# Kernel tuning notes

Hardware: AMD Instinct MI355X
Metric: run time of the kernel (lower is better)

## Reference

```python
import jax, jax.numpy as jnp
import numpy as np

N = 512        # n_t (sequence length of observations)
D_IN = 128     # input feature dim
PROJ = 128     # proj_dim
ENC = 128      # enc_dim
H = 4          # num_head
E = PROJ // H  # per-head dim = 32
SCALE = 1.0 / np.float32(np.sqrt(E))


def setup_inputs() -> dict:
    key = jax.random.key(0)
    ks = jax.random.split(key, 14)
    g = lambda k, sh: (jax.random.normal(k, sh, jnp.float32) * 0.05)
    inp = jax.random.normal(ks[0], (N, D_IN), jnp.float32)
    # irregular observation times, sorted ascending
    pos = jnp.sort(jax.random.uniform(ks[1], (N,), jnp.float32) * 100.0)
    # PosEncodingBlock frequency vector f: exp(arange(0,enc,2) * -(ln(10000)/enc))
    f = jnp.exp(jnp.arange(0, ENC, 2, dtype=jnp.float32) * (-(np.log(10000.0) / ENC)))
    return {
        "inp": inp, "pos": pos, "f": f,
        "Wq": g(ks[2], (D_IN, PROJ)), "bq": g(ks[3], (PROJ,)),
        "Wk": g(ks[4], (D_IN, PROJ)), "bk": g(ks[5], (PROJ,)),
        "Wv": g(ks[6], (D_IN, PROJ)), "bv": g(ks[7], (PROJ,)),
        "Wqt": g(ks[8], (D_IN, PROJ)), "bqt": g(ks[9], (PROJ,)),
        "Wt": g(ks[10], (ENC, PROJ)), "bt": g(ks[11], (PROJ,)),
    }


def _heads(x):
    # 'n (h e) -> h n e'
    return x.reshape(N, H, E).transpose(1, 0, 2)


def reference(inp, pos, f, Wq, bq, Wk, bk, Wv, bv, Wqt, bqt, Wt, bt):
    q = _heads(inp @ Wq + bq)   # (h, n, e)
    k = _heads(inp @ Wk + bk)
    v = _heads(inp @ Wv + bv)
    qt = _heads(inp @ Wqt + bqt)

    score = jnp.einsum('hne,hme->hnm', q, k) * SCALE  # (h, n, n)

    # Equivariant relative-time positional encoding: (n, n, ENC)
    rel_time = pos[:, None] - pos[None, :]                    # (n, n)
    angles = rel_time[..., None] * f                          # (n, n, ENC/2)
    # rearrange([sin, cos], 'z t l k -> t l (k z)') interleaves sin/cos per freq
    pos_enc = jnp.stack([jnp.sin(angles), jnp.cos(angles)], axis=-1).reshape(N, N, ENC)

    # time_dense then 'n1 n2 (h e) -> h n1 n2 e'
    t = (pos_enc @ Wt + bt).reshape(N, N, H, E).transpose(2, 0, 1, 3)  # (h, n, n, e)
    # tf.linalg.matvec(t, q_t): bias[h,i,j] = sum_e t[h,i,j,e] * qt[h,i,e]
    score = score + jnp.einsum('hnme,hne->hnm', t, qt) * SCALE

    mask = jnp.tril(jnp.ones((N, N), dtype=bool))
    score = jnp.where(mask, score, -jnp.inf)
    weight = jax.nn.softmax(score, axis=-1)
    weight = jnp.where(mask, weight, 0.0)
    # dropout is identity at inference

    out = jnp.einsum('hnm,hme->hne', weight, v)  # (h, n, e)
    return out.transpose(1, 0, 2).reshape(N, PROJ)  # 'h n e -> n (h e)'
```

## Files before the change

### kernel.cpp

```cpp
#include <hip/hip_runtime.h>
#include <math.h>

namespace {
constexpr int N = 512;
constexpr int DIN = 128;
constexpr int PROJ = 128;
constexpr int H = 4;
constexpr int E = 32;
constexpr int KF = 64;
constexpr int FEAT = E + 2*KF;
constexpr float SCALE = 0.17677669529663687f;
constexpr int TI = 8;
constexpr int JQ = 8;
constexpr int CHUNK = 64;
}

__device__ __forceinline__ float wave_max(float v) {
  #pragma unroll
  for (int o = 32; o > 0; o >>= 1) v = fmaxf(v, __shfl_xor(v, o, 64));
  return v;
}
__device__ __forceinline__ float wave_sum(float v) {
  #pragma unroll
  for (int o = 32; o > 0; o >>= 1) v += __shfl_xor(v, o, 64);
  return v;
}

__global__ __launch_bounds__(256)
void proj_feat_kernel(const float* __restrict__ inp,
                      const float* __restrict__ pos, const float* __restrict__ f,
                      const float* __restrict__ Wq, const float* __restrict__ bq,
                      const float* __restrict__ Wk, const float* __restrict__ bk,
                      const float* __restrict__ Wv, const float* __restrict__ bv,
                      const float* __restrict__ Wqt, const float* __restrict__ bqt,
                      const float* __restrict__ Wt, const float* __restrict__ bt,
                      float* __restrict__ Afeat, float* __restrict__ BTk,
                      float* __restrict__ Vmat, float* __restrict__ Btrig,
                      float* __restrict__ c0)
{
  const int bx = blockIdx.x;
  const int t = threadIdx.x;
  const int c = t & 127;

  if (bx < 384) {
    const int mat = bx >> 7, rowTile = bx & 127;
    const int i0 = rowTile * 4;
    const int half = t >> 7;
    __shared__ float x[4][DIN];
    #pragma unroll
    for (int r = 0; r < 2; ++r) {
      const int id = t + r * 256;
      x[id >> 7][id & 127] = inp[i0 * DIN + id];
    }
    const float* W; const float* bvec;
    switch (mat) {
      case 0:  W = Wq; bvec = bq; break;
      case 1:  W = Wk; bvec = bk; break;
      default: W = Wv; bvec = bv; break;
    }
    __syncthreads();
    const int r0 = half * 2, r1 = r0 + 1;
    float a0 = 0.f, a1 = 0.f;
    #pragma unroll 8
    for (int d = 0; d < DIN; d += 2) {
      const float w0 = W[d * PROJ + c];
      const float w1 = W[(d + 1) * PROJ + c];
      const float2 x0 = *(const float2*)&x[r0][d];
      const float2 x1 = *(const float2*)&x[r1][d];
      a0 += w0 * x0.x + w1 * x0.y;
      a1 += w0 * x1.x + w1 * x1.y;
    }
    const float bb = bvec[c];
    a0 += bb; a1 += bb;
    const int h = c >> 5, e = c & 31;
    const int row0 = i0 + r0, row1 = i0 + r1;
    if (mat == 0) {
      Afeat[(h * N + row0) * FEAT + e] = a0;
      Afeat[(h * N + row1) * FEAT + e] = a1;
    } else if (mat == 1) {
      BTk[(size_t)(h * E + e) * N + row0] = a0;
      BTk[(size_t)(h * E + e) * N + row1] = a1;
    } else {
      Vmat[(h * N + row0) * E + e] = a0;
      Vmat[(h * N + row1) * E + e] = a1;
    }
    return;
  }

  const int i0 = (bx - 384) * 2;
  const int r = t >> 7;
  __shared__ float x[2][DIN];
  __shared__ float qt_l[2][PROJ];
  __shared__ float ss[2][KF], sc[2][KF];
  __shared__ float ul[2][H][PROJ];

  x[r][c] = inp[i0 * DIN + t];
  if (t < 128) {
    const int rr = t >> 6, k = t & 63;
    float s_, c_;
    sincosf(pos[i0 + rr] * f[k], &s_, &c_);
    ss[rr][k] = s_; sc[rr][k] = c_;
  }
  __syncthreads();

  {
    float a = 0.f;
    #pragma unroll 8
    for (int d = 0; d < DIN; d += 2) {
      const float w0 = Wqt[d * PROJ + c];
      const float w1 = Wqt[(d + 1) * PROJ + c];
      const float2 xv = *(const float2*)&x[r][d];
      a += w0 * xv.x + w1 * xv.y;
    }
    qt_l[r][c] = a + bqt[c];
  }
  __syncthreads();

  {
    const int g = t >> 7;
    const float* wrow = &Wt[c * PROJ];
    #pragma unroll
    for (int hh = 2 * g; hh < 2 * g + 2; ++hh) {
      float uA = 0.f, uB = 0.f;
      #pragma unroll
      for (int e4 = 0; e4 < E; e4 += 4) {
        const float4 w = *(const float4*)&wrow[hh * E + e4];
        const float4 qA = *(const float4*)&qt_l[0][hh * E + e4];
        const float4 qB = *(const float4*)&qt_l[1][hh * E + e4];
        uA += w.x * qA.x + w.y * qA.y + w.z * qA.z + w.w * qA.w;
        uB += w.x * qB.x + w.y * qB.y + w.z * qB.z + w.w * qB.w;
      }
      ul[0][hh][c] = uA;
      ul[1][hh][c] = uB;
    }
  }
  if (t < 8) {
    const int rr = t & 1, hh = t >> 1;
    float acc = 0.f;
    for (int e2 = 0; e2 < E; ++e2) acc += bt[hh * E + e2] * qt_l[rr][hh * E + e2];
    c0[hh * N + i0 + rr] = acc;
  }
  __syncthreads();

  {
    const int k = t & 63, hh = t >> 6;
    #pragma unroll
    for (int rr = 0; rr < 2; ++rr) {
      const float u0 = ul[rr][hh][2 * k], u1 = ul[rr][hh][2 * k + 1];
      const float s_ = ss[rr][k], c_ = sc[rr][k];
      Afeat[(hh * N + i0 + rr) * FEAT + E + k]      =  u0 * s_ + u1 * c_;
      Afeat[(hh * N + i0 + rr) * FEAT + E + KF + k] = -u0 * c_ + u1 * s_;
      if (hh == 0) {
        Btrig[k * N + i0 + rr]        = c_;
        Btrig[(KF + k) * N + i0 + rr] = s_;
      }
    }
  }
}

__global__ __launch_bounds__(256, 4)
void attn_partial(const float* __restrict__ Afeat, const float* __restrict__ BTk,
                  const float* __restrict__ Btrig, const float* __restrict__ Vmat,
                  const float* __restrict__ c0,
                  float* __restrict__ Po, float* __restrict__ Pm,
                  float* __restrict__ Ps)
{
  const int b = blockIdx.x, h = blockIdx.y, q = blockIdx.z;
  const int i0 = b * TI, jbase = q * CHUNK;
  if (jbase > i0) return;
  const int t = threadIdx.x;
  const int lane = t & 63;
  const int rh = __builtin_amdgcn_readfirstlane(t >> 6);
  const int j = jbase + lane;

  __shared__ float pT[CHUNK][12];
  __shared__ float obuf[16][TI][32];

  const float* A0 = Afeat + (size_t)(h * N + i0 + rh * 2) * FEAT;
  const float* A1 = A0 + FEAT;
  const float cc0 = c0[h * N + i0 + rh * 2];
  const float cc1 = c0[h * N + i0 + rh * 2 + 1];

  float acc0 = 0.f, acc1 = 0.f;
  {
    const float* Bk = BTk + (size_t)h * E * N + j;
    const float* Bt = Btrig + j;
    #pragma unroll
    for (int bb = 0; bb < 10; ++bb) {
      const float* src = (bb < 2) ? (Bk + (size_t)(bb * 16) * N)
                                  : (Bt + (size_t)((bb - 2) * 16) * N);
      const int aoff = 16 * bb;
      float bv[16];
      #pragma unroll
      for (int dd = 0; dd < 16; ++dd) bv[dd] = src[(size_t)dd * N];
      #pragma unroll
      for (int dd = 0; dd < 16; dd += 4) {
        const float4 a0 = *(const float4*)&A0[aoff + dd];
        const float4 a1 = *(const float4*)&A1[aoff + dd];
        acc0 += a0.x * bv[dd] + a0.y * bv[dd+1] + a0.z * bv[dd+2] + a0.w * bv[dd+3];
        acc1 += a1.x * bv[dd] + a1.y * bv[dd+1] + a1.z * bv[dd+2] + a1.w * bv[dd+3];
      }
    }
  }

  const int i_0 = i0 + rh * 2, i_1 = i_0 + 1;
  const float s0 = (j <= i_0) ? (acc0 + cc0) * SCALE : -INFINITY;
  const float s1 = (j <= i_1) ? (acc1 + cc1) * SCALE : -INFINITY;

  const float m0 = wave_max(s0);
  const float m1 = wave_max(s1);
  const float p0 = __expf(s0 - m0);
  const float p1 = __expf(s1 - m1);
  const float sum0 = wave_sum(p0);
  const float sum1 = wave_sum(p1);

  *(float2*)&pT[lane][rh * 2] = make_float2(p0, p1);
  if (lane == 0) {
    const int base = (h * N + i_0) * JQ + q;
    Pm[base]      = m0; Ps[base]      = sum0;
    Pm[base + JQ] = m1; Ps[base + JQ] = sum1;
  }
  __syncthreads();

  const int e2 = (t & 15) * 2, gg = t >> 4;
  float2 o[TI];
  #pragma unroll
  for (int r = 0; r < TI; ++r) o[r] = make_float2(0.f, 0.f);
  const float* Vh = Vmat + ((size_t)h * N + jbase) * E + e2;
  #pragma unroll
  for (int it = 0; it < CHUNK / 16; ++it) {
    const int jl = gg + 16 * it;
    const float2 vv = *(const float2*)&Vh[jl * E];
    const float4 pa = *(const float4*)&pT[jl][0];
    const float4 pb = *(const float4*)&pT[jl][4];
    o[0].x += pa.x * vv.x; o[0].y += pa.x * vv.y;
    o[1].x += pa.y * vv.x; o[1].y += pa.y * vv.y;
    o[2].x += pa.z * vv.x; o[2].y += pa.z * vv.y;
    o[3].x += pa.w * vv.x; o[3].y += pa.w * vv.y;
    o[4].x += pb.x * vv.x; o[4].y += pb.x * vv.y;
    o[5].x += pb.y * vv.x; o[5].y += pb.y * vv.y;
    o[6].x += pb.z * vv.x; o[6].y += pb.z * vv.y;
    o[7].x += pb.w * vv.x; o[7].y += pb.w * vv.y;
  }
  #pragma unroll
  for (int r = 0; r < TI; ++r) *(float2*)&obuf[gg][r][e2] = o[r];
  __syncthreads();
  {
    const int r = t >> 5, e = t & 31;
    float tot = 0.f;
    #pragma unroll
    for (int g2 = 0; g2 < 16; ++g2) tot += obuf[g2][r][e];
    Po[((size_t)(h * N + i0 + r) * JQ + q) * E + e] = tot;
  }
}

__global__ __launch_bounds__(256)
void attn_combine(const float* __restrict__ Po, const float* __restrict__ Pm,
                  const float* __restrict__ Ps, float* __restrict__ out)
{
  const int gid = blockIdx.x * 256 + threadIdx.x;
  const int task = gid >> 5, e = gid & 31;
  const int h = task >> 9, i = task & (N - 1);
  const int nq = (i >> 6) + 1;
  float m = -INFINITY;
  for (int qq = 0; qq < nq; ++qq) m = fmaxf(m, Pm[task * JQ + qq]);
  float s = 0.f, o = 0.f;
  for (int qq = 0; qq < nq; ++qq) {
    const float w = __expf(Pm[task * JQ + qq] - m);
    s += Ps[task * JQ + qq] * w;
    o += Po[(size_t)(task * JQ + qq) * E + e] * w;
  }
  out[i * PROJ + h * E + e] = o / s;
}

extern "C" void kernel_launch(void* const* d_in, const int* in_sizes, int n_in,
                              void* d_out, int out_size, void* d_ws, size_t ws_size,
                              hipStream_t stream) {
  const float* inp = (const float*)d_in[0];
  const float* pos = (const float*)d_in[1];
  const float* f   = (const float*)d_in[2];
  const float* Wq  = (const float*)d_in[3];
  const float* bq  = (const float*)d_in[4];
  const float* Wk  = (const float*)d_in[5];
  const float* bk  = (const float*)d_in[6];
  const float* Wv  = (const float*)d_in[7];
  const float* bv  = (const float*)d_in[8];
  const float* Wqt = (const float*)d_in[9];
  const float* bqt = (const float*)d_in[10];
  const float* Wt  = (const float*)d_in[11];
  const float* bt  = (const float*)d_in[12];
  float* out = (float*)d_out;

  float* ws    = (float*)d_ws;
  float* Afeat = ws;
  float* BTk   = Afeat + H * N * FEAT;
  float* Btrig = BTk + (size_t)H * E * N;
  float* Vmat  = Btrig + 2 * KF * N;
  float* c0    = Vmat + H * N * E;
  float* Po    = c0 + H * N;
  float* Pm    = Po + (size_t)H * N * JQ * E;
  float* Ps    = Pm + H * N * JQ;

  proj_feat_kernel<<<640, 256, 0, stream>>>(inp, pos, f, Wq, bq, Wk, bk, Wv, bv,
                                            Wqt, bqt, Wt, bt,
                                            Afeat, BTk, Vmat, Btrig, c0);
  attn_partial<<<dim3(N / TI, H, JQ), 256, 0, stream>>>(Afeat, BTk, Btrig, Vmat,
                                                        c0, Po, Pm, Ps);
  attn_combine<<<H * N * E / 256, 256, 0, stream>>>(Po, Pm, Ps, out);
}
```

Baseline: 30.64 us.

## Split score dot product over feature segments per wave and merge B features

Each wave in the score phase now covers all 8 query rows over one quarter of the 160-wide feature dimension instead of 2 rows over the full dimension. The partial sums are reduced through shared memory. The K and trig feature tables are merged into one per-head Bfeat buffer, so each B element loaded from global memory is reused across 8 rows instead of 2. The trig rows are now duplicated per head, which adds workspace and writes. The change also adds a sync and LDS traffic and drops the occupancy hint from launch bounds.

```diff
diff --git a/kernel.cpp b/kernel.cpp
--- a/kernel.cpp
+++ b/kernel.cpp
@@ -13,6 +13,7 @@
 constexpr int TI = 8;
 constexpr int JQ = 8;
 constexpr int CHUNK = 64;
+constexpr int FSEG = FEAT / 4;
 }
 
 __device__ __forceinline__ float wave_max(float v) {
@@ -34,9 +35,8 @@
                       const float* __restrict__ Wv, const float* __restrict__ bv,
                       const float* __restrict__ Wqt, const float* __restrict__ bqt,
                       const float* __restrict__ Wt, const float* __restrict__ bt,
-                      float* __restrict__ Afeat, float* __restrict__ BTk,
-                      float* __restrict__ Vmat, float* __restrict__ Btrig,
-                      float* __restrict__ c0)
+                      float* __restrict__ Afeat, float* __restrict__ Bfeat,
+                      float* __restrict__ Vmat, float* __restrict__ c0)
 {
   const int bx = blockIdx.x;
   const int t = threadIdx.x;
@@ -78,8 +78,8 @@
       Afeat[(h * N + row0) * FEAT + e] = a0;
       Afeat[(h * N + row1) * FEAT + e] = a1;
     } else if (mat == 1) {
-      BTk[(size_t)(h * E + e) * N + row0] = a0;
-      BTk[(size_t)(h * E + e) * N + row1] = a1;
+      Bfeat[(size_t)(h * FEAT + e) * N + row0] = a0;
+      Bfeat[(size_t)(h * FEAT + e) * N + row1] = a1;
     } else {
       Vmat[(h * N + row0) * E + e] = a0;
       Vmat[(h * N + row1) * E + e] = a1;
@@ -150,18 +150,15 @@
       const float s_ = ss[rr][k], c_ = sc[rr][k];
       Afeat[(hh * N + i0 + rr) * FEAT + E + k]      =  u0 * s_ + u1 * c_;
       Afeat[(hh * N + i0 + rr) * FEAT + E + KF + k] = -u0 * c_ + u1 * s_;
-      if (hh == 0) {
-        Btrig[k * N + i0 + rr]        = c_;
-        Btrig[(KF + k) * N + i0 + rr] = s_;
-      }
-    }
-  }
-}
-
-__global__ __launch_bounds__(256, 4)
-void attn_partial(const float* __restrict__ Afeat, const float* __restrict__ BTk,
-                  const float* __restrict__ Btrig, const float* __restrict__ Vmat,
-                  const float* __restrict__ c0,
+      Bfeat[(size_t)(hh * FEAT + E + k) * N + i0 + rr]      = c_;
+      Bfeat[(size_t)(hh * FEAT + E + KF + k) * N + i0 + rr] = s_;
+    }
+  }
+}
+
+__global__ __launch_bounds__(256)
+void attn_partial(const float* __restrict__ Afeat, const float* __restrict__ Bfeat,
+                  const float* __restrict__ Vmat, const float* __restrict__ c0,
                   float* __restrict__ Po, float* __restrict__ Pm,
                   float* __restrict__ Ps)
 {
@@ -170,42 +167,46 @@
   if (jbase > i0) return;
   const int t = threadIdx.x;
   const int lane = t & 63;
-  const int rh = __builtin_amdgcn_readfirstlane(t >> 6);
+  const int w = __builtin_amdgcn_readfirstlane(t >> 6);
   const int j = jbase + lane;
 
+  __shared__ float pacc[4][TI][65];
   __shared__ float pT[CHUNK][12];
   __shared__ float obuf[16][TI][32];
 
-  const float* A0 = Afeat + (size_t)(h * N + i0 + rh * 2) * FEAT;
-  const float* A1 = A0 + FEAT;
-  const float cc0 = c0[h * N + i0 + rh * 2];
-  const float cc1 = c0[h * N + i0 + rh * 2 + 1];
-
-  float acc0 = 0.f, acc1 = 0.f;
-  {
-    const float* Bk = BTk + (size_t)h * E * N + j;
-    const float* Bt = Btrig + j;
-    #pragma unroll
-    for (int bb = 0; bb < 10; ++bb) {
-      const float* src = (bb < 2) ? (Bk + (size_t)(bb * 16) * N)
-                                  : (Bt + (size_t)((bb - 2) * 16) * N);
-      const int aoff = 16 * bb;
-      float bv[16];
+  {
+    const float* Arow = Afeat + (size_t)(h * N + i0) * FEAT + FSEG * w;
+    const float* Bp   = Bfeat + ((size_t)h * FEAT + FSEG * w) * N + j;
+    float acc[TI];
+    #pragma unroll
+    for (int r = 0; r < TI; ++r) acc[r] = 0.f;
+    #pragma unroll
+    for (int dd = 0; dd < FSEG; dd += 4) {
+      const float b0 = Bp[(size_t)(dd + 0) * N];
+      const float b1 = Bp[(size_t)(dd + 1) * N];
+      const float b2 = Bp[(size_t)(dd + 2) * N];
+      const float b3 = Bp[(size_t)(dd + 3) * N];
       #pragma unroll
-      for (int dd = 0; dd < 16; ++dd) bv[dd] = src[(size_t)dd * N];
-      #pragma unroll
-      for (int dd = 0; dd < 16; dd += 4) {
-        const float4 a0 = *(const float4*)&A0[aoff + dd];
-        const float4 a1 = *(const float4*)&A1[aoff + dd];
-        acc0 += a0.x * bv[dd] + a0.y * bv[dd+1] + a0.z * bv[dd+2] + a0.w * bv[dd+3];
-        acc1 += a1.x * bv[dd] + a1.y * bv[dd+1] + a1.z * bv[dd+2] + a1.w * bv[dd+3];
+      for (int r = 0; r < TI; ++r) {
+        const float4 a = *(const float4*)&Arow[r * FEAT + dd];
+        acc[r] += a.x * b0 + a.y * b1 + a.z * b2 + a.w * b3;
       }
     }
-  }
-
-  const int i_0 = i0 + rh * 2, i_1 = i_0 + 1;
-  const float s0 = (j <= i_0) ? (acc0 + cc0) * SCALE : -INFINITY;
-  const float s1 = (j <= i_1) ? (acc1 + cc1) * SCALE : -INFINITY;
+    #pragma unroll
+    for (int r = 0; r < TI; ++r) pacc[w][r][lane] = acc[r];
+  }
+  __syncthreads();
+
+  const int i_0 = i0 + 2 * w, i_1 = i_0 + 1;
+  const float cc0 = c0[h * N + i_0];
+  const float cc1 = c0[h * N + i_1];
+  const float d0 = pacc[0][2 * w][lane] + pacc[1][2 * w][lane]
+                 + pacc[2][2 * w][lane] + pacc[3][2 * w][lane];
+  const float d1 = pacc[0][2 * w + 1][lane] + pacc[1][2 * w + 1][lane]
+                 + pacc[2][2 * w + 1][lane] + pacc[3][2 * w + 1][lane];
+
+  const float s0 = (j <= i_0) ? (d0 + cc0) * SCALE : -INFINITY;
+  const float s1 = (j <= i_1) ? (d1 + cc1) * SCALE : -INFINITY;
 
   const float m0 = wave_max(s0);
   const float m1 = wave_max(s1);
@@ -214,7 +215,7 @@
   const float sum0 = wave_sum(p0);
   const float sum1 = wave_sum(p1);
 
-  *(float2*)&pT[lane][rh * 2] = make_float2(p0, p1);
+  *(float2*)&pT[lane][w * 2] = make_float2(p0, p1);
   if (lane == 0) {
     const int base = (h * N + i_0) * JQ + q;
     Pm[base]      = m0; Ps[base]      = sum0;
@@ -293,9 +294,8 @@
 
   float* ws    = (float*)d_ws;
   float* Afeat = ws;
-  float* BTk   = Afeat + H * N * FEAT;
-  float* Btrig = BTk + (size_t)H * E * N;
-  float* Vmat  = Btrig + 2 * KF * N;
+  float* Bfeat = Afeat + H * N * FEAT;
+  float* Vmat  = Bfeat + (size_t)H * FEAT * N;
   float* c0    = Vmat + H * N * E;
   float* Po    = c0 + H * N;
   float* Pm    = Po + (size_t)H * N * JQ * E;
@@ -303,8 +303,8 @@
 
   proj_feat_kernel<<<640, 256, 0, stream>>>(inp, pos, f, Wq, bq, Wk, bk, Wv, bv,
                                             Wqt, bqt, Wt, bt,
-                                            Afeat, BTk, Vmat, Btrig, c0);
-  attn_partial<<<dim3(N / TI, H, JQ), 256, 0, stream>>>(Afeat, BTk, Btrig, Vmat,
+                                            Afeat, Bfeat, Vmat, c0);
+  attn_partial<<<dim3(N / TI, H, JQ), 256, 0, stream>>>(Afeat, Bfeat, Vmat,
                                                         c0, Po, Pm, Ps);
   attn_combine<<<H * N * E / 256, 256, 0, stream>>>(Po, Pm, Ps, out);
 }
```

After: 28.42 us. -7.3%, faster.
